# Optimization experiments

Hardware: AMD Instinct MI355X
Metric: run time of the kernel (lower is better)

The kernel has to match this reference:

```python
import jax, jax.numpy as jnp
import numpy as np

D_MODEL = 1024
N_HEADS = 16
HEAD_DIM = D_MODEL // N_HEADS
WINDOW = 128  # radius w; attend to [i-w, i+w]


def setup_inputs() -> dict:
    key = jax.random.key(0)
    ks = jax.random.split(key, 5)
    scale = 1.0 / np.sqrt(D_MODEL)
    x = jax.random.normal(ks[0], (2, 2048, D_MODEL), dtype=jnp.float32)
    # nn.MultiheadAttention packed projections
    in_proj_w = jax.random.normal(ks[1], (3 * D_MODEL, D_MODEL), dtype=jnp.float32) * scale
    in_proj_b = jnp.zeros((3 * D_MODEL,), dtype=jnp.float32)
    out_w = jax.random.normal(ks[2], (D_MODEL, D_MODEL), dtype=jnp.float32) * scale
    out_b = jnp.zeros((D_MODEL,), dtype=jnp.float32)
    return {"x": x, "in_proj_w": in_proj_w, "in_proj_b": in_proj_b,
            "out_w": out_w, "out_b": out_b}


def reference(x, in_proj_w, in_proj_b, out_w, out_b):
    B, S, D = x.shape
    H, Dh = N_HEADS, HEAD_DIM
    # packed qkv projection (PyTorch: x @ W^T + b)
    qkv = x @ in_proj_w.T + in_proj_b              # [B, S, 3D]
    q, k, v = jnp.split(qkv, 3, axis=-1)
    q = q.reshape(B, S, H, Dh)
    k = k.reshape(B, S, H, Dh)
    v = v.reshape(B, S, H, Dh)
    scores = jnp.einsum('bqhd,bkhd->bhqk', q, k) / np.sqrt(Dh)  # [B,H,S,S]
    # window mask: allowed iff |i - j| <= WINDOW
    idx = jnp.arange(S)
    allowed = jnp.abs(idx[:, None] - idx[None, :]) <= WINDOW    # [S, S]
    scores = jnp.where(allowed[None, None], scores, -jnp.inf)
    attn = jax.nn.softmax(scores, axis=-1)
    out = jnp.einsum('bhqk,bkhd->bqhd', attn, v).reshape(B, S, D)
    return out @ out_w.T + out_b
```

## Files before the change

### kernel.cpp

```cpp
#include <hip/hip_runtime.h>
#include <hip/hip_bf16.h>


#define S_LEN 2048
#define NH 16
#define DH 64
#define DM 1024
#define WIN 128
#define K_DIM 1024

typedef __attribute__((ext_vector_type(8))) short short8;
typedef __attribute__((ext_vector_type(4))) short short4_t;
typedef __attribute__((ext_vector_type(4))) float f32x4;
typedef __attribute__((ext_vector_type(16))) float f32x16;

__device__ __forceinline__ unsigned short f2bf(float f){
  unsigned u = __float_as_uint(f);
  u += 0x7fffu + ((u >> 16) & 1u);
  return (unsigned short)(u >> 16);
}
__device__ __forceinline__ unsigned pk2(float lo, float hi){
  __hip_bfloat162 h = __float22bfloat162_rn(float2{lo, hi});
  return *reinterpret_cast<unsigned*>(&h);
}
__device__ __forceinline__ void async16(void* l, const void* g){
  __builtin_amdgcn_global_load_lds((const __attribute__((address_space(1))) void*)g,
                                   (__attribute__((address_space(3))) void*)l, 16, 0, 0);
}

__global__ void cvt_all(const float* __restrict__ x, const float* __restrict__ w1,
                        const float* __restrict__ wo,
                        short* __restrict__ xb, short* __restrict__ w1b,
                        short* __restrict__ wob){
  int b = blockIdx.x;
  const float* src; short* dst; int base;
  if (b < 4096)      { src = x;  dst = xb;  base = b; }
  else if (b < 7168) { src = w1; dst = w1b; base = b - 4096; }
  else               { src = wo; dst = wob; base = b - 7168; }
  int i = (base * 256 + threadIdx.x) * 4;
  float4 v = *(const float4*)(src + i);
  short4_t o;
  o.x = (short)f2bf(v.x); o.y = (short)f2bf(v.y);
  o.z = (short)f2bf(v.z); o.w = (short)f2bf(v.w);
  *(short4_t*)(dst + i) = o;
}

__global__ __launch_bounds__(256) void gemm_qkv(
    const short* __restrict__ A, const short* __restrict__ Bw,
    const float* __restrict__ bias,
    short* __restrict__ Qb, short* __restrict__ Kb, short* __restrict__ Vb)
{
  __shared__ short As[128*64], Bs[128*64];
  int tid = threadIdx.x;
  int lane = tid & 63, wv = tid >> 6;
  int wr = wv >> 1, wc = wv & 1;
  int lr = lane & 15, lh = lane >> 4;
  int m0 = blockIdx.y * 128, n0 = blockIdx.x * 128;

  f32x4 acc[4][4] = {};
  for (int kt = 0; kt < K_DIM; kt += 64) {
    #pragma unroll
    for (int j = 0; j < 4; ++j) {
      int off = j*256 + tid;
      int lrow = off >> 3, slin = off & 7;
      int sg = slin ^ (lrow & 7);
      async16(&As[lrow*64 + slin*8], A  + (size_t)(m0+lrow)*K_DIM + kt + sg*8);
      async16(&Bs[lrow*64 + slin*8], Bw + (size_t)(n0+lrow)*K_DIM + kt + sg*8);
    }
    __syncthreads();
    short8 af[4][2], bfr[4][2];
    #pragma unroll
    for (int m = 0; m < 4; ++m)
      #pragma unroll
      for (int kk = 0; kk < 2; ++kk)
        af[m][kk]  = *(const short8*)&As[(wr*64 + m*16 + lr)*64 + (((kk*4 + lh) ^ (lr & 7))*8)];
    #pragma unroll
    for (int n = 0; n < 4; ++n)
      #pragma unroll
      for (int kk = 0; kk < 2; ++kk)
        bfr[n][kk] = *(const short8*)&Bs[(wc*64 + n*16 + lr)*64 + (((kk*4 + lh) ^ (lr & 7))*8)];
    #pragma unroll
    for (int m = 0; m < 4; ++m)
      #pragma unroll
      for (int n = 0; n < 4; ++n)
        #pragma unroll
        for (int kk = 0; kk < 2; ++kk)
          acc[m][n] = __builtin_amdgcn_mfma_f32_16x16x32_bf16(af[m][kk], bfr[n][kk], acc[m][n], 0, 0, 0);
    __syncthreads();
  }
  #pragma unroll
  for (int m = 0; m < 4; ++m) {
    #pragma unroll
    for (int n = 0; n < 4; ++n) {
      int col = n0 + wc*64 + n*16 + lr;
      float bv = bias[col];
      int which = col >> 10, cc = col & 1023;
      int h = cc >> 6, d = cc & 63;
      float scl = which == 0 ? 0.125f : 1.0f;
      int growb = m0 + wr*64 + m*16 + lh*4;
      int b = growb >> 11, s0 = growb & 2047;
      if (which == 2) {
        short4_t vv;
        vv.x = (short)f2bf(acc[m][n][0] + bv);
        vv.y = (short)f2bf(acc[m][n][1] + bv);
        vv.z = (short)f2bf(acc[m][n][2] + bv);
        vv.w = (short)f2bf(acc[m][n][3] + bv);
        *(short4_t*)&Vb[((size_t)(b*NH + h)*DH + d)*S_LEN + s0] = vv;
      } else {
        short* dst = which == 0 ? Qb : Kb;
        #pragma unroll
        for (int r = 0; r < 4; ++r) {
          float v = (acc[m][n][r] + bv) * scl;
          dst[(((size_t)b*NH + h)*S_LEN + s0 + r)*DH + d] = (short)f2bf(v);
        }
      }
    }
  }
}

__global__ __launch_bounds__(512) void gemm_out(
    const short* __restrict__ A, const short* __restrict__ Bw,
    const float* __restrict__ bias, float* __restrict__ Out)
{
  __shared__ short As[128*64], Bs[128*64];
  int tid = threadIdx.x;
  int lane = tid & 63, wv = tid >> 6;
  int wr = wv >> 2, wc = wv & 3;
  int lr = lane & 15, lh = lane >> 4;
  int m0 = blockIdx.y * 128, n0 = blockIdx.x * 128;

  f32x4 acc[4][2] = {};
  for (int kt = 0; kt < K_DIM; kt += 64) {
    #pragma unroll
    for (int j = 0; j < 2; ++j) {
      int off = j*512 + tid;
      int lrow = off >> 3, slin = off & 7;
      int sg = slin ^ (lrow & 7);
      async16(&As[lrow*64 + slin*8], A  + (size_t)(m0+lrow)*K_DIM + kt + sg*8);
      async16(&Bs[lrow*64 + slin*8], Bw + (size_t)(n0+lrow)*K_DIM + kt + sg*8);
    }
    __syncthreads();
    short8 af[4][2], bfr[2][2];
    #pragma unroll
    for (int m = 0; m < 4; ++m)
      #pragma unroll
      for (int kk = 0; kk < 2; ++kk)
        af[m][kk]  = *(const short8*)&As[(wr*64 + m*16 + lr)*64 + (((kk*4 + lh) ^ (lr & 7))*8)];
    #pragma unroll
    for (int n = 0; n < 2; ++n)
      #pragma unroll
      for (int kk = 0; kk < 2; ++kk)
        bfr[n][kk] = *(const short8*)&Bs[(wc*32 + n*16 + lr)*64 + (((kk*4 + lh) ^ (lr & 7))*8)];
    #pragma unroll
    for (int m = 0; m < 4; ++m)
      #pragma unroll
      for (int n = 0; n < 2; ++n)
        #pragma unroll
        for (int kk = 0; kk < 2; ++kk)
          acc[m][n] = __builtin_amdgcn_mfma_f32_16x16x32_bf16(af[m][kk], bfr[n][kk], acc[m][n], 0, 0, 0);
    __syncthreads();
  }
  #pragma unroll
  for (int m = 0; m < 4; ++m) {
    #pragma unroll
    for (int n = 0; n < 2; ++n) {
      int col = n0 + wc*32 + n*16 + lr;
      float bv = bias[col];
      #pragma unroll
      for (int r = 0; r < 4; ++r) {
        int grow = m0 + wr*64 + m*16 + lh*4 + r;
        Out[(size_t)grow*DM + col] = acc[m][n][r] + bv;
      }
    }
  }
}

__global__ __launch_bounds__(256) void attn_mfma(
    const short* __restrict__ Qb, const short* __restrict__ Kb,
    const short* __restrict__ VTb, short* __restrict__ Ob)
{
  int tid = threadIdx.x;
  int lane = tid & 63, wv = tid >> 6;
  int q31 = lane & 31, h2 = lane >> 5;
  int bh = blockIdx.y;
  int q0w = blockIdx.x * 128 + wv * 32;
  int qa = q0w + q31;

  const short* Qg = Qb  + (size_t)bh * S_LEN * DH;
  const short* Kg = Kb  + (size_t)bh * S_LEN * DH;
  const short* Vg = VTb + (size_t)bh * DH * S_LEN;

  short8 qf[4];
  #pragma unroll
  for (int kc = 0; kc < 4; ++kc)
    qf[kc] = *(const short8*)(Qg + (size_t)qa * DH + kc*16 + h2*8);

  int ks = q0w - WIN; if (ks < 0) ks = 0;
  int ke = q0w + 32 + WIN; if (ke > S_LEN) ke = S_LEN;

  f32x16 o0 = {}, o1 = {};
  float m = -1e37f, l = 0.f;

  for (int t0 = ks; t0 < ke; t0 += 32) {
    f32x16 s = {};
    #pragma unroll
    for (int kc = 0; kc < 4; ++kc) {
      short8 kf = *(const short8*)(Kg + (size_t)(t0 + q31) * DH + kc*16 + h2*8);
      s = __builtin_amdgcn_mfma_f32_32x32x16_bf16(kf, qf[kc], s, 0, 0, 0);
    }
    float p[16];
    float tm = -1e38f;
    #pragma unroll
    for (int r = 0; r < 16; ++r) {
      int key = t0 + (r & 3) + 8*(r >> 2) + 4*h2;
      bool ok = (key >= qa - WIN) && (key <= qa + WIN);
      p[r] = ok ? s[r] : -1e38f;
      tm = fmaxf(tm, p[r]);
    }
    tm = fmaxf(tm, __shfl_xor(tm, 32, 64));
    float mn = fmaxf(m, tm);
    float sc = __expf(m - mn);
    float ts = 0.f;
    #pragma unroll
    for (int r = 0; r < 16; ++r) { p[r] = __expf(p[r] - mn); ts += p[r]; }
    ts += __shfl_xor(ts, 32, 64);
    l = l * sc + ts;
    m = mn;
    #pragma unroll
    for (int r = 0; r < 16; ++r) { o0[r] *= sc; o1[r] *= sc; }

    #pragma unroll
    for (int kc2 = 0; kc2 < 2; ++kc2) {
      unsigned A1 = pk2(p[kc2*8+0], p[kc2*8+1]);
      unsigned A2 = pk2(p[kc2*8+2], p[kc2*8+3]);
      unsigned B1 = pk2(p[kc2*8+4], p[kc2*8+5]);
      unsigned B2 = pk2(p[kc2*8+6], p[kc2*8+7]);
      unsigned sA1 = (unsigned)__shfl_xor((int)A1, 32, 64);
      unsigned sA2 = (unsigned)__shfl_xor((int)A2, 32, 64);
      unsigned sB1 = (unsigned)__shfl_xor((int)B1, 32, 64);
      unsigned sB2 = (unsigned)__shfl_xor((int)B2, 32, 64);
      union { unsigned u[4]; short8 v; } pa;
      pa.u[0] = h2 ? sB1 : A1;
      pa.u[1] = h2 ? sB2 : A2;
      pa.u[2] = h2 ? B1 : sA1;
      pa.u[3] = h2 ? B2 : sA2;
      #pragma unroll
      for (int mt = 0; mt < 2; ++mt) {
        short8 vf = *(const short8*)(Vg + (size_t)(mt*32 + q31) * S_LEN + t0 + kc2*16 + h2*8);
        if (mt == 0) o0 = __builtin_amdgcn_mfma_f32_32x32x16_bf16(vf, pa.v, o0, 0, 0, 0);
        else         o1 = __builtin_amdgcn_mfma_f32_32x32x16_bf16(vf, pa.v, o1, 0, 0, 0);
      }
    }
  }

  float inv = 1.0f / l;
  int b = bh >> 4, hh = bh & 15;
  unsigned* Orow = (unsigned*)Ob + ((size_t)b*S_LEN + qa) * (DM/2) + hh*32;
  #pragma unroll
  for (int mt = 0; mt < 2; ++mt) {
    #pragma unroll
    for (int aa = 0; aa < 4; ++aa) {
      #pragma unroll
      for (int e = 0; e < 2; ++e) {
        int r = 4*aa + 2*e;
        float x0 = (mt ? o1[r]   : o0[r])   * inv;
        float x1 = (mt ? o1[r+1] : o0[r+1]) * inv;
        int d = 2*e + 8*aa + 4*h2 + 32*mt;
        Orow[d >> 1] = pk2(x0, x1);
      }
    }
  }
}

extern "C" void kernel_launch(void* const* d_in, const int* in_sizes, int n_in,
                              void* d_out, int out_size, void* d_ws, size_t ws_size,
                              hipStream_t stream) {
  const float* x  = (const float*)d_in[0];
  const float* w1 = (const float*)d_in[1];
  const float* b1 = (const float*)d_in[2];
  const float* wo = (const float*)d_in[3];
  const float* bo = (const float*)d_in[4];
  float* out = (float*)d_out;

  char* ws = (char*)d_ws;
  short* xb  = (short*)(ws);
  short* w1b = (short*)(ws + (size_t)8*1024*1024);
  short* wob = (short*)(ws + (size_t)14*1024*1024);
  short* Qb  = (short*)(ws + (size_t)16*1024*1024);
  short* Kb  = (short*)(ws + (size_t)24*1024*1024);
  short* VTb = (short*)(ws + (size_t)32*1024*1024);
  short* Ab  = (short*)(ws + (size_t)40*1024*1024);

  cvt_all<<<dim3(8192), dim3(256), 0, stream>>>(x, w1, wo, xb, w1b, wob);
  gemm_qkv<<<dim3(24, 32), dim3(256), 0, stream>>>(xb, w1b, b1, Qb, Kb, VTb);
  attn_mfma<<<dim3(16, 32), dim3(256), 0, stream>>>(Qb, Kb, VTb, Ab);
  gemm_out<<<dim3(8, 32), dim3(512), 0, stream>>>(Ab, wob, bo, out);
}
```

Before: 171.3 us.

## Retile output GEMM to 128x64 with block swizzle; hoist loads and set MFMA priority in attention

The output projection GEMM moves from 128x128 tiles with 512 threads to 128x64 tiles with 256 threads. The grid doubles to 512 blocks, and block ids are remapped so neighbouring blocks share A rows for better L2 reuse and finer balance across CUs. In the attention kernel, K and V fragment loads are hoisted ahead of their MFMA sequences, which are wrapped in s_setprio to favour matrix issue across waves. The smaller tiles mean more redundant loads of A per block.

```diff
diff --git a/kernel.cpp b/kernel.cpp
--- a/kernel.cpp
+++ b/kernel.cpp
@@ -118,25 +118,34 @@
   }
 }
 
-__global__ __launch_bounds__(512) void gemm_out(
+__global__ __launch_bounds__(256) void gemm_out(
     const short* __restrict__ A, const short* __restrict__ Bw,
     const float* __restrict__ bias, float* __restrict__ Out)
 {
-  __shared__ short As[128*64], Bs[128*64];
+  __shared__ short As[128*64], Bs[64*64];
   int tid = threadIdx.x;
   int lane = tid & 63, wv = tid >> 6;
-  int wr = wv >> 2, wc = wv & 3;
+  int wr = wv >> 1, wc = wv & 1;
   int lr = lane & 15, lh = lane >> 4;
-  int m0 = blockIdx.y * 128, n0 = blockIdx.x * 128;
+  int bid = blockIdx.x + blockIdx.y * 16;
+  int swz = (bid & 7) * 64 + (bid >> 3);
+  int nt = swz & 15, mt = swz >> 4;
+  int m0 = mt * 128, n0 = nt * 64;
 
   f32x4 acc[4][2] = {};
   for (int kt = 0; kt < K_DIM; kt += 64) {
     #pragma unroll
-    for (int j = 0; j < 2; ++j) {
-      int off = j*512 + tid;
+    for (int j = 0; j < 4; ++j) {
+      int off = j*256 + tid;
       int lrow = off >> 3, slin = off & 7;
       int sg = slin ^ (lrow & 7);
-      async16(&As[lrow*64 + slin*8], A  + (size_t)(m0+lrow)*K_DIM + kt + sg*8);
+      async16(&As[lrow*64 + slin*8], A + (size_t)(m0+lrow)*K_DIM + kt + sg*8);
+    }
+    #pragma unroll
+    for (int j = 0; j < 2; ++j) {
+      int off = j*256 + tid;
+      int lrow = off >> 3, slin = off & 7;
+      int sg = slin ^ (lrow & 7);
       async16(&Bs[lrow*64 + slin*8], Bw + (size_t)(n0+lrow)*K_DIM + kt + sg*8);
     }
     __syncthreads();
@@ -202,12 +211,16 @@
   float m = -1e37f, l = 0.f;
 
   for (int t0 = ks; t0 < ke; t0 += 32) {
+    short8 kf[4];
+    #pragma unroll
+    for (int kc = 0; kc < 4; ++kc)
+      kf[kc] = *(const short8*)(Kg + (size_t)(t0 + q31) * DH + kc*16 + h2*8);
     f32x16 s = {};
-    #pragma unroll
-    for (int kc = 0; kc < 4; ++kc) {
-      short8 kf = *(const short8*)(Kg + (size_t)(t0 + q31) * DH + kc*16 + h2*8);
-      s = __builtin_amdgcn_mfma_f32_32x32x16_bf16(kf, qf[kc], s, 0, 0, 0);
-    }
+    __builtin_amdgcn_s_setprio(1);
+    #pragma unroll
+    for (int kc = 0; kc < 4; ++kc)
+      s = __builtin_amdgcn_mfma_f32_32x32x16_bf16(kf[kc], qf[kc], s, 0, 0, 0);
+    __builtin_amdgcn_s_setprio(0);
     float p[16];
     float tm = -1e38f;
     #pragma unroll
@@ -244,12 +257,12 @@
       pa.u[1] = h2 ? sB2 : A2;
       pa.u[2] = h2 ? B1 : sA1;
       pa.u[3] = h2 ? B2 : sA2;
-      #pragma unroll
-      for (int mt = 0; mt < 2; ++mt) {
-        short8 vf = *(const short8*)(Vg + (size_t)(mt*32 + q31) * S_LEN + t0 + kc2*16 + h2*8);
-        if (mt == 0) o0 = __builtin_amdgcn_mfma_f32_32x32x16_bf16(vf, pa.v, o0, 0, 0, 0);
-        else         o1 = __builtin_amdgcn_mfma_f32_32x32x16_bf16(vf, pa.v, o1, 0, 0, 0);
-      }
+      short8 vf0 = *(const short8*)(Vg + (size_t)q31 * S_LEN + t0 + kc2*16 + h2*8);
+      short8 vf1 = *(const short8*)(Vg + (size_t)(32 + q31) * S_LEN + t0 + kc2*16 + h2*8);
+      __builtin_amdgcn_s_setprio(1);
+      o0 = __builtin_amdgcn_mfma_f32_32x32x16_bf16(vf0, pa.v, o0, 0, 0, 0);
+      o1 = __builtin_amdgcn_mfma_f32_32x32x16_bf16(vf1, pa.v, o1, 0, 0, 0);
+      __builtin_amdgcn_s_setprio(0);
     }
   }
 
@@ -294,5 +307,5 @@
   cvt_all<<<dim3(8192), dim3(256), 0, stream>>>(x, w1, wo, xb, w1b, wob);
   gemm_qkv<<<dim3(24, 32), dim3(256), 0, stream>>>(xb, w1b, b1, Qb, Kb, VTb);
   attn_mfma<<<dim3(16, 32), dim3(256), 0, stream>>>(Qb, Kb, VTb, Ab);
-  gemm_out<<<dim3(8, 32), dim3(512), 0, stream>>>(Ab, wob, bo, out);
-}
+  gemm_out<<<dim3(16, 32), dim3(256), 0, stream>>>(Ab, wob, bo, out);
+}
```

Measured after the change: 168.2 us. No clear change (-1.8%).
